# Kernel optimization log

Measured on AMD Instinct MI355X. Metric: run time of the kernel, lower is better.

Reference implementation:

```python
import jax, jax.numpy as jnp
import numpy as np

D_MODEL = 1024
N_HEADS = 16
HEAD_DIM = D_MODEL // N_HEADS  # 64
BASE = 10000.0
MAX_X, MAX_Y, MAX_Z = 32, 32, 8
NEG_INF = -1e9  # stand-in for float('-inf') in masked_fill; identical after softmax


def _split_dims(head_dim):
    n_pairs = head_dim // 2
    px = n_pairs // 3
    py = n_pairs // 3
    pz = n_pairs - px - py
    return px * 2, py * 2, pz * 2


def _cos_sin_table(dim, max_pos):
    # matches RotaryEmbedding3D._register_cache
    inv_freq = 1.0 / (BASE ** (np.arange(0, dim, 2, dtype=np.float32) / dim))
    t = np.arange(max_pos, dtype=np.float32)[:, None] * inv_freq  # [max_pos, dim/2]
    cos = np.repeat(np.cos(t), 2, axis=-1)  # repeat_interleave(2)
    sin = np.repeat(np.sin(t), 2, axis=-1)
    return jnp.asarray(cos), jnp.asarray(sin)


def _rotate_half(x):
    x1 = x[..., ::2]
    x2 = x[..., 1::2]
    return jnp.stack((-x2, x1), axis=-1).reshape(x.shape)


def setup_inputs() -> dict:
    key = jax.random.key(0)
    k1, k2, k3, k4, k5, k6 = jax.random.split(key, 6)
    B, S = 2, 2048
    hidden_states = jax.random.normal(k1, (B, S, D_MODEL), dtype=jnp.float32)
    w_qkv = jax.random.normal(k2, (D_MODEL, 3 * D_MODEL), dtype=jnp.float32) * 0.02
    w_out = jax.random.normal(k3, (D_MODEL, D_MODEL), dtype=jnp.float32) * 0.02
    px = jax.random.randint(k4, (B, S, 1), 0, MAX_X)
    py = jax.random.randint(k5, (B, S, 1), 0, MAX_Y)
    pz = jax.random.randint(k6, (B, S, 1), 0, MAX_Z)
    pos_xyz = jnp.concatenate([px, py, pz], axis=-1).astype(jnp.int64)
    causal_mask = jnp.triu(jnp.ones((S, S), dtype=bool), k=1)[None, None]  # [1,1,S,S]
    return {"hidden_states": hidden_states, "w_qkv": w_qkv, "w_out": w_out,
            "pos_xyz": pos_xyz, "causal_mask": causal_mask}


def reference(hidden_states, w_qkv, w_out, pos_xyz, causal_mask):
    B, S, D = hidden_states.shape
    H, Hd = N_HEADS, HEAD_DIM
    # fused QKV projection
    qkv = hidden_states @ w_qkv  # [B,S,3D]
    qkv = qkv.reshape(B, S, 3, H, Hd).transpose(2, 0, 3, 1, 4)  # [3,B,H,S,Hd]
    q, k, v = qkv[0], qkv[1], qkv[2]
    # 3D RoPE tables and lookups
    dx, dy, dz = _split_dims(Hd)
    cx, sx = _cos_sin_table(dx, MAX_X)
    cy, sy = _cos_sin_table(dy, MAX_Y)
    cz, sz = _cos_sin_table(dz, MAX_Z)
    ix = jnp.clip(pos_xyz[..., 0], 0, MAX_X - 1)
    iy = jnp.clip(pos_xyz[..., 1], 0, MAX_Y - 1)
    iz = jnp.clip(pos_xyz[..., 2], 0, MAX_Z - 1)
    cos = jnp.concatenate([cx[ix], cy[iy], cz[iz]], axis=-1)[:, None]  # [B,1,S,Hd]
    sin = jnp.concatenate([sx[ix], sy[iy], sz[iz]], axis=-1)[:, None]
    q = q * cos + _rotate_half(q) * sin
    k = k * cos + _rotate_half(k) * sin
    # SDPA with causal bias
    scale = Hd ** -0.5
    scores = jnp.einsum('bhqd,bhkd->bhqk', q, k) * scale
    scores = jnp.where(causal_mask, jnp.asarray(NEG_INF, scores.dtype), scores)
    probs = jax.nn.softmax(scores, axis=-1)
    attn = jnp.einsum('bhqk,bhkd->bhqd', probs, v)
    attn = attn.transpose(0, 2, 1, 3).reshape(B, S, D)
    return attn @ w_out
```

## Files before the change

### kernel.cpp

```cpp
#include <hip/hip_runtime.h>
#include <hip/hip_bf16.h>
#include <math.h>

typedef __bf16 bf16;
typedef __bf16 bf16x4 __attribute__((ext_vector_type(4)));
typedef __bf16 bf16x8 __attribute__((ext_vector_type(8)));
typedef float f32x4 __attribute__((ext_vector_type(4)));
typedef int i32x4 __attribute__((ext_vector_type(4)));

#define SEQ 2048
#define NHEADS 16
#define HDIM 64
#define DM 1024
#define QKVW 3072

__device__ __forceinline__ void gload_lds16(const void* g, void* l) {
  __builtin_amdgcn_global_load_lds(
      (const __attribute__((address_space(1))) unsigned int*)g,
      (__attribute__((address_space(3))) unsigned int*)l, 16, 0, 0);
}

__device__ __forceinline__ int pk2(float a, float b) {
  union { __bf16 h; unsigned short u; } ua, ub;
  ua.h = (__bf16)a; ub.h = (__bf16)b;
  return (int)ua.u | ((int)ub.u << 16);
}

__global__ __launch_bounds__(256) void prep(
    const float* __restrict__ hidden, const float* __restrict__ w_qkv,
    const float* __restrict__ w_out, const int* __restrict__ pos,
    bf16* __restrict__ hid_bf, bf16* __restrict__ wqkvT,
    bf16* __restrict__ woutT, float2* __restrict__ tbl) {
  __shared__ float tile[64][65];
  int idx = blockIdx.x, tid = threadIdx.x;
  if (idx < 2048) {
    int i = (idx * 256 + tid) * 8;
    float4 a = *(const float4*)(hidden + i);
    float4 b = *(const float4*)(hidden + i + 4);
    bf16x8 o;
    o[0] = (bf16)a.x; o[1] = (bf16)a.y; o[2] = (bf16)a.z; o[3] = (bf16)a.w;
    o[4] = (bf16)b.x; o[5] = (bf16)b.y; o[6] = (bf16)b.z; o[7] = (bf16)b.w;
    *(bf16x8*)(hid_bf + i) = o;
  } else if (idx < 3072) {
    const float* in; bf16* out; int R, C, t;
    if (idx < 2816) { t = idx - 2048; in = w_qkv; out = wqkvT; R = 1024; C = 3072; }
    else            { t = idx - 2816; in = w_out; out = woutT; R = 1024; C = 1024; }
    int nbx = C >> 6;
    int c0 = (t % nbx) * 64, r0 = (t / nbx) * 64;
    int col = tid & 63, rb = (tid >> 6) * 16;
#pragma unroll
    for (int i = 0; i < 16; ++i)
      tile[rb + i][col] = in[(size_t)(r0 + rb + i) * C + c0 + col];
    __syncthreads();
#pragma unroll
    for (int i = 0; i < 16; ++i)
      out[(size_t)(c0 + rb + i) * R + r0 + col] = (bf16)tile[col][rb + i];
  } else {
    const float LN1E4 = 9.210340371976184f;
    int gi = (idx - 3072) * 256 + tid;
    int m = gi >> 5, pr = gi & 31;
    int axis, d, iloc;
    if (pr < 10)      { axis = 0; d = 20; iloc = pr; }
    else if (pr < 20) { axis = 1; d = 20; iloc = pr - 10; }
    else              { axis = 2; d = 24; iloc = pr - 20; }
    int p = pos[m * 3 + axis];
    int pmax = (axis == 2) ? 7 : 31;
    p = p < 0 ? 0 : (p > pmax ? pmax : p);
    float invf = __expf(-((float)(2 * iloc) / (float)d) * LN1E4);
    float sn, cs;
    __sincosf((float)p * invf, &sn, &cs);
    tbl[gi] = make_float2(cs, sn);
  }
}

__global__ __launch_bounds__(256) void post_qkv(
    bf16* __restrict__ qkv, const float2* __restrict__ tbl,
    bf16* __restrict__ vT) {
  __shared__ bf16 btile[64][65];
  int idx = blockIdx.x, tid = threadIdx.x;
  if (idx < 2048) {
    int gi = idx * 256 + tid;
    int m = gi >> 7, seg = gi & 127;
    bf16* p = qkv + (size_t)m * QKVW + seg * 16;
    bf16x8 a = *(const bf16x8*)p;
    bf16x8 b2 = *(const bf16x8*)(p + 8);
    const float2* t = tbl + m * 32 + (((seg * 16) & 63) >> 1);
#pragma unroll
    for (int j = 0; j < 4; ++j) {
      float2 cs = t[j];
      float e = (float)a[2 * j], o = (float)a[2 * j + 1];
      a[2 * j]     = (bf16)(e * cs.x - o * cs.y);
      a[2 * j + 1] = (bf16)(o * cs.x + e * cs.y);
    }
#pragma unroll
    for (int j = 0; j < 4; ++j) {
      float2 cs = t[4 + j];
      float e = (float)b2[2 * j], o = (float)b2[2 * j + 1];
      b2[2 * j]     = (bf16)(e * cs.x - o * cs.y);
      b2[2 * j + 1] = (bf16)(o * cs.x + e * cs.y);
    }
    *(bf16x8*)p = a;
    *(bf16x8*)(p + 8) = b2;
  } else {
    int t = idx - 2048;
    int s0 = (t & 31) * 64, bh = t >> 5;
    int b = bh >> 4, h = bh & 15;
    const bf16* src = qkv + (size_t)(b * SEQ + s0) * QKVW + 2 * DM + h * 64;
    int col = tid & 63, rb = (tid >> 6) * 16;
#pragma unroll
    for (int i = 0; i < 16; ++i)
      btile[rb + i][col] = src[(size_t)(rb + i) * QKVW + col];
    __syncthreads();
    bf16* dst = vT + (size_t)bh * HDIM * SEQ + s0;
#pragma unroll
    for (int i = 0; i < 16; ++i)
      dst[(size_t)(rb + i) * SEQ + col] = btile[col][rb + i];
  }
}

__global__ __launch_bounds__(256) void gemm_bt(
    const bf16* __restrict__ A, const bf16* __restrict__ Bt,
    bf16* __restrict__ C, int M, int N, int K) {
  __shared__ __align__(16) bf16 a_lds[128 * 32];
  __shared__ __align__(16) bf16 b_lds[128 * 32];
  int tid = threadIdx.x;
  int wave = tid >> 6, lane = tid & 63;
  int quad = lane >> 4, l15 = lane & 15;
  int wm = wave >> 1, wn = wave & 1;

  int flat = blockIdx.y * gridDim.x + blockIdx.x;
  int mband = gridDim.y >> 3;
  int xcd = flat & 7, sidx = flat >> 3;
  int m0 = (xcd * mband + (sidx % mband)) * 128;
  int n0 = (sidx / mband) * 128;

  f32x4 acc[4][4] = {};

  for (int kt = 0; kt < K; kt += 32) {
    __syncthreads();
#pragma unroll
    for (int call = 0; call < 2; ++call) {
      int chunk = call * 256 + tid;
      int row = chunk >> 2, cc = (chunk & 3) * 8;
      gload_lds16(A + (size_t)(m0 + row) * K + kt + cc,
                  (char*)a_lds + call * 4096 + wave * 1024);
      gload_lds16(Bt + (size_t)(n0 + row) * K + kt + cc,
                  (char*)b_lds + call * 4096 + wave * 1024);
    }
    __syncthreads();
    bf16x8 af[4], bfr[4];
#pragma unroll
    for (int i = 0; i < 4; ++i) {
      af[i]  = *(const bf16x8*)(a_lds + (wm * 64 + i * 16 + l15) * 32 + quad * 8);
      bfr[i] = *(const bf16x8*)(b_lds + (wn * 64 + i * 16 + l15) * 32 + quad * 8);
    }
#pragma unroll
    for (int mi = 0; mi < 4; ++mi)
#pragma unroll
      for (int ni = 0; ni < 4; ++ni)
        acc[mi][ni] = __builtin_amdgcn_mfma_f32_16x16x32_bf16(
            af[mi], bfr[ni], acc[mi][ni], 0, 0, 0);
  }

#pragma unroll
  for (int mi = 0; mi < 4; ++mi) {
    int mb = m0 + wm * 64 + mi * 16 + quad * 4;
#pragma unroll
    for (int ni = 0; ni < 4; ++ni) {
      int n = n0 + wn * 64 + ni * 16 + l15;
#pragma unroll
      for (int r = 0; r < 4; ++r)
        C[(size_t)(mb + r) * N + n] = (bf16)acc[mi][ni][r];
    }
  }
}

__global__ __launch_bounds__(256) void gemm_bt64(
    const bf16* __restrict__ A, const bf16* __restrict__ Bt,
    float* __restrict__ C, int M, int N, int K) {
  __shared__ __align__(16) bf16 a_lds[64 * 32];
  __shared__ __align__(16) bf16 b_lds[128 * 32];
  int tid = threadIdx.x;
  int wave = tid >> 6, lane = tid & 63;
  int quad = lane >> 4, l15 = lane & 15;
  int wm = wave >> 1, wn = wave & 1;

  int flat = blockIdx.y * gridDim.x + blockIdx.x;
  int mband = gridDim.y >> 3;
  int xcd = flat & 7, sidx = flat >> 3;
  int m0 = (xcd * mband + (sidx % mband)) * 64;
  int n0 = (sidx / mband) * 128;

  f32x4 acc[2][4] = {};

  for (int kt = 0; kt < K; kt += 32) {
    __syncthreads();
    {
      int row = tid >> 2, cc = (tid & 3) * 8;
      gload_lds16(A + (size_t)(m0 + row) * K + kt + cc,
                  (char*)a_lds + wave * 1024);
    }
#pragma unroll
    for (int call = 0; call < 2; ++call) {
      int chunk = call * 256 + tid;
      int row = chunk >> 2, cc = (chunk & 3) * 8;
      gload_lds16(Bt + (size_t)(n0 + row) * K + kt + cc,
                  (char*)b_lds + call * 4096 + wave * 1024);
    }
    __syncthreads();
    bf16x8 af[2], bfr[4];
#pragma unroll
    for (int i = 0; i < 2; ++i)
      af[i] = *(const bf16x8*)(a_lds + (wm * 32 + i * 16 + l15) * 32 + quad * 8);
#pragma unroll
    for (int i = 0; i < 4; ++i)
      bfr[i] = *(const bf16x8*)(b_lds + (wn * 64 + i * 16 + l15) * 32 + quad * 8);
#pragma unroll
    for (int mi = 0; mi < 2; ++mi)
#pragma unroll
      for (int ni = 0; ni < 4; ++ni)
        acc[mi][ni] = __builtin_amdgcn_mfma_f32_16x16x32_bf16(
            af[mi], bfr[ni], acc[mi][ni], 0, 0, 0);
  }

#pragma unroll
  for (int mi = 0; mi < 2; ++mi) {
    int mb = m0 + wm * 32 + mi * 16 + quad * 4;
#pragma unroll
    for (int ni = 0; ni < 4; ++ni) {
      int n = n0 + wn * 64 + ni * 16 + l15;
#pragma unroll
      for (int r = 0; r < 4; ++r)
        C[(size_t)(mb + r) * N + n] = acc[mi][ni][r];
    }
  }
}

__global__ __launch_bounds__(256) void attn_fwd(
    const bf16* __restrict__ QKV, const bf16* __restrict__ VT,
    bf16* __restrict__ O) {
  __shared__ __align__(16) bf16 k_lds[2][64 * 72];
  __shared__ __align__(16) bf16 v_lds[2][64 * 72];
  const float C2 = 0.18033688011112042f;
  const float C3 = -5.770780163555854f;
  int tid = threadIdx.x;
  int wave = tid >> 6, lane = tid & 63;
  int quad = lane >> 4, l15 = lane & 15;
  int idx = blockIdx.x;
  int bh = idx & 31;
  int g = idx >> 5;
  int qt = (g < 16) ? (31 - g) : (g - 16);
  int q0 = qt * 64;
  int b = bh >> 4, h = bh & 15;
  const bf16* Qb = QKV + (size_t)b * SEQ * QKVW + h * 64;
  const bf16* Kb = Qb + DM;
  const bf16* VTb = VT + (size_t)bh * HDIM * SEQ;

  int qg = q0 + wave * 16 + l15;
  const bf16* qr = Qb + (size_t)qg * QKVW;
  bf16x8 qf0 = *(const bf16x8*)(qr + quad * 8);
  bf16x8 qf1 = *(const bf16x8*)(qr + 32 + quad * 8);

  int r0c = tid >> 3, off0 = (tid & 7) * 8;

  int niter = qt + 1;
  f32x4 oT[4] = {};
  float lsum = 0.f;

  bf16x8 kpre0 = *(const bf16x8*)(Kb + (size_t)r0c * QKVW + off0);
  bf16x8 kpre1 = *(const bf16x8*)(Kb + (size_t)(r0c + 32) * QKVW + off0);
  bf16x8 vpre0 = *(const bf16x8*)(VTb + (size_t)r0c * SEQ + off0);
  bf16x8 vpre1 = *(const bf16x8*)(VTb + (size_t)(r0c + 32) * SEQ + off0);

  for (int tkv = 0; tkv < niter; ++tkv) {
    int kv0 = tkv * 64;
    bf16* kb = k_lds[tkv & 1];
    bf16* vb = v_lds[tkv & 1];
    *(bf16x8*)(kb + r0c * 72 + off0) = kpre0;
    *(bf16x8*)(kb + (r0c + 32) * 72 + off0) = kpre1;
    *(bf16x8*)(vb + r0c * 72 + off0) = vpre0;
    *(bf16x8*)(vb + (r0c + 32) * 72 + off0) = vpre1;
    __syncthreads();
    if (tkv + 1 < niter) {
      int kn = kv0 + 64;
      kpre0 = *(const bf16x8*)(Kb + (size_t)(kn + r0c) * QKVW + off0);
      kpre1 = *(const bf16x8*)(Kb + (size_t)(kn + r0c + 32) * QKVW + off0);
      vpre0 = *(const bf16x8*)(VTb + (size_t)r0c * SEQ + kn + off0);
      vpre1 = *(const bf16x8*)(VTb + (size_t)(r0c + 32) * SEQ + kn + off0);
    }
    f32x4 sT[4];
    __builtin_amdgcn_s_setprio(1);
#pragma unroll
    for (int nt = 0; nt < 4; ++nt) {
      const bf16* kr = kb + (nt * 16 + l15) * 72;
      bf16x8 kf0 = *(const bf16x8*)(kr + quad * 8);
      bf16x8 kf1 = *(const bf16x8*)(kr + 32 + quad * 8);
      f32x4 z = {};
      z = __builtin_amdgcn_mfma_f32_16x16x32_bf16(kf0, qf0, z, 0, 0, 0);
      z = __builtin_amdgcn_mfma_f32_16x16x32_bf16(kf1, qf1, z, 0, 0, 0);
      sT[nt] = z;
    }
    __builtin_amdgcn_s_setprio(0);
    float pv[4][4];
    if (tkv == qt) {
#pragma unroll
      for (int nt = 0; nt < 4; ++nt)
#pragma unroll
        for (int r = 0; r < 4; ++r) {
          float p = __builtin_amdgcn_exp2f(sT[nt][r] * C2 + C3);
          int kvg = kv0 + nt * 16 + 4 * quad + r;
          if (kvg > qg) p = 0.f;
          pv[nt][r] = p;
          lsum += p;
        }
    } else {
#pragma unroll
      for (int nt = 0; nt < 4; ++nt)
#pragma unroll
        for (int r = 0; r < 4; ++r) {
          float p = __builtin_amdgcn_exp2f(sT[nt][r] * C2 + C3);
          pv[nt][r] = p;
          lsum += p;
        }
    }
    i32x4 w0 = {pk2(pv[0][0], pv[0][1]), pk2(pv[0][2], pv[0][3]),
                pk2(pv[1][0], pv[1][1]), pk2(pv[1][2], pv[1][3])};
    i32x4 w1 = {pk2(pv[2][0], pv[2][1]), pk2(pv[2][2], pv[2][3]),
                pk2(pv[3][0], pv[3][1]), pk2(pv[3][2], pv[3][3])};
    bf16x8 pa0 = __builtin_bit_cast(bf16x8, w0);
    bf16x8 pa1 = __builtin_bit_cast(bf16x8, w1);
    __builtin_amdgcn_s_setprio(1);
#pragma unroll
    for (int dt = 0; dt < 4; ++dt) {
      const bf16* vd = vb + (dt * 16 + l15) * 72 + 4 * quad;
      bf16x4 a0 = *(const bf16x4*)(vd);
      bf16x4 a1 = *(const bf16x4*)(vd + 16);
      bf16x8 vf0 = __builtin_shufflevector(a0, a1, 0, 1, 2, 3, 4, 5, 6, 7);
      oT[dt] = __builtin_amdgcn_mfma_f32_16x16x32_bf16(pa0, vf0, oT[dt], 0, 0, 0);
      bf16x4 b0 = *(const bf16x4*)(vd + 32);
      bf16x4 b1 = *(const bf16x4*)(vd + 48);
      bf16x8 vf1 = __builtin_shufflevector(b0, b1, 0, 1, 2, 3, 4, 5, 6, 7);
      oT[dt] = __builtin_amdgcn_mfma_f32_16x16x32_bf16(pa1, vf1, oT[dt], 0, 0, 0);
    }
    __builtin_amdgcn_s_setprio(0);
  }
  float t = lsum;
  t += __shfl_xor(t, 16);
  t += __shfl_xor(t, 32);
#pragma unroll
  for (int r = 0; r < 4; ++r) {
    float Lr = __shfl(t, 4 * quad + r);
    float inv = 1.f / Lr;
    int sq = q0 + wave * 16 + 4 * quad + r;
#pragma unroll
    for (int dt = 0; dt < 4; ++dt)
      O[(size_t)(b * SEQ + sq) * DM + h * HDIM + dt * 16 + l15] =
          (bf16)(oT[dt][r] * inv);
  }
}

extern "C" void kernel_launch(void* const* d_in, const int* in_sizes, int n_in,
                              void* d_out, int out_size, void* d_ws,
                              size_t ws_size, hipStream_t stream) {
  const float* hidden = (const float*)d_in[0];
  const float* w_qkv  = (const float*)d_in[1];
  const float* w_out  = (const float*)d_in[2];
  const int*   pos    = (const int*)d_in[3];
  float* out = (float*)d_out;

  char* ws = (char*)d_ws;
  bf16* wqkvT  = (bf16*)ws;  ws += (size_t)3072 * 1024 * 2;
  bf16* woutT  = (bf16*)ws;  ws += (size_t)1024 * 1024 * 2;
  bf16* hid_bf = (bf16*)ws;  ws += (size_t)4096 * 1024 * 2;
  bf16* qkv_ws = (bf16*)ws;  ws += (size_t)4096 * 3072 * 2;
  bf16* vT_ws  = (bf16*)ws;  ws += (size_t)32 * SEQ * HDIM * 2;
  float2* ropetbl = (float2*)ws;
  bf16* attn_ws = hid_bf;

  prep<<<dim3(3584), 256, 0, stream>>>(hidden, w_qkv, w_out, pos,
                                       hid_bf, wqkvT, woutT, ropetbl);
  gemm_bt<<<dim3(24, 32), 256, 0, stream>>>(
      hid_bf, wqkvT, qkv_ws, 4096, 3072, 1024);
  post_qkv<<<dim3(3072), 256, 0, stream>>>(qkv_ws, ropetbl, vT_ws);
  attn_fwd<<<dim3(1024), 256, 0, stream>>>(qkv_ws, vT_ws, attn_ws);
  gemm_bt64<<<dim3(8, 64), 256, 0, stream>>>(
      attn_ws, woutT, out, 4096, 1024, 1024);
}
```

Measured before the change: 196.1 us.

## Fuse RoPE and V transpose into QKV GEMM epilogue

Removes the separate post_qkv kernel and applies the rotary embedding inside the QKV GEMM epilogue. Paired elements are exchanged with a lane shuffle, and V tiles are written directly in transposed layout as 4-wide bf16 vectors. This saves one launch and a full read and rewrite of the Q/K region plus the V transpose pass. The epilogue becomes heavier: there are per-element table loads, and the transposed stores are strided. RoPE is now applied to fp32 accumulators before the bf16 rounding instead of after it.

```diff
diff --git a/kernel.cpp b/kernel.cpp
--- a/kernel.cpp
+++ b/kernel.cpp
@@ -73,54 +73,10 @@
   }
 }
 
-__global__ __launch_bounds__(256) void post_qkv(
-    bf16* __restrict__ qkv, const float2* __restrict__ tbl,
-    bf16* __restrict__ vT) {
-  __shared__ bf16 btile[64][65];
-  int idx = blockIdx.x, tid = threadIdx.x;
-  if (idx < 2048) {
-    int gi = idx * 256 + tid;
-    int m = gi >> 7, seg = gi & 127;
-    bf16* p = qkv + (size_t)m * QKVW + seg * 16;
-    bf16x8 a = *(const bf16x8*)p;
-    bf16x8 b2 = *(const bf16x8*)(p + 8);
-    const float2* t = tbl + m * 32 + (((seg * 16) & 63) >> 1);
-#pragma unroll
-    for (int j = 0; j < 4; ++j) {
-      float2 cs = t[j];
-      float e = (float)a[2 * j], o = (float)a[2 * j + 1];
-      a[2 * j]     = (bf16)(e * cs.x - o * cs.y);
-      a[2 * j + 1] = (bf16)(o * cs.x + e * cs.y);
-    }
-#pragma unroll
-    for (int j = 0; j < 4; ++j) {
-      float2 cs = t[4 + j];
-      float e = (float)b2[2 * j], o = (float)b2[2 * j + 1];
-      b2[2 * j]     = (bf16)(e * cs.x - o * cs.y);
-      b2[2 * j + 1] = (bf16)(o * cs.x + e * cs.y);
-    }
-    *(bf16x8*)p = a;
-    *(bf16x8*)(p + 8) = b2;
-  } else {
-    int t = idx - 2048;
-    int s0 = (t & 31) * 64, bh = t >> 5;
-    int b = bh >> 4, h = bh & 15;
-    const bf16* src = qkv + (size_t)(b * SEQ + s0) * QKVW + 2 * DM + h * 64;
-    int col = tid & 63, rb = (tid >> 6) * 16;
-#pragma unroll
-    for (int i = 0; i < 16; ++i)
-      btile[rb + i][col] = src[(size_t)(rb + i) * QKVW + col];
-    __syncthreads();
-    bf16* dst = vT + (size_t)bh * HDIM * SEQ + s0;
-#pragma unroll
-    for (int i = 0; i < 16; ++i)
-      dst[(size_t)(rb + i) * SEQ + col] = btile[col][rb + i];
-  }
-}
-
-__global__ __launch_bounds__(256) void gemm_bt(
+__global__ __launch_bounds__(256) void gemm_qkv(
     const bf16* __restrict__ A, const bf16* __restrict__ Bt,
-    bf16* __restrict__ C, int M, int N, int K) {
+    bf16* __restrict__ C, const float2* __restrict__ tbl,
+    bf16* __restrict__ vT, int M, int N, int K) {
   __shared__ __align__(16) bf16 a_lds[128 * 32];
   __shared__ __align__(16) bf16 b_lds[128 * 32];
   int tid = threadIdx.x;
@@ -162,15 +118,40 @@
             af[mi], bfr[ni], acc[mi][ni], 0, 0, 0);
   }
 
-#pragma unroll
-  for (int mi = 0; mi < 4; ++mi) {
-    int mb = m0 + wm * 64 + mi * 16 + quad * 4;
-#pragma unroll
-    for (int ni = 0; ni < 4; ++ni) {
-      int n = n0 + wn * 64 + ni * 16 + l15;
-#pragma unroll
-      for (int r = 0; r < 4; ++r)
-        C[(size_t)(mb + r) * N + n] = (bf16)acc[mi][ni][r];
+  if (n0 >= 2048) {
+    int b = m0 >> 11;
+#pragma unroll
+    for (int mi = 0; mi < 4; ++mi) {
+      int mb = m0 + wm * 64 + mi * 16 + quad * 4;
+      int s0 = mb - b * 2048;
+#pragma unroll
+      for (int ni = 0; ni < 4; ++ni) {
+        int n = n0 + wn * 64 + ni * 16 + l15;
+        int hv = (n - 2048) >> 6, d = n & 63;
+        bf16x4 v4;
+#pragma unroll
+        for (int r = 0; r < 4; ++r) v4[r] = (bf16)acc[mi][ni][r];
+        *(bf16x4*)(vT + ((size_t)(b * 16 + hv) * HDIM + d) * SEQ + s0) = v4;
+      }
+    }
+  } else {
+#pragma unroll
+    for (int mi = 0; mi < 4; ++mi) {
+      int mb = m0 + wm * 64 + mi * 16 + quad * 4;
+#pragma unroll
+      for (int ni = 0; ni < 4; ++ni) {
+        int n = n0 + wn * 64 + ni * 16 + l15;
+        int pr = (n & 63) >> 1;
+        float sgn = (n & 1) ? 1.f : -1.f;
+#pragma unroll
+        for (int r = 0; r < 4; ++r) {
+          float own = acc[mi][ni][r];
+          float par = __shfl_xor(own, 1);
+          int m = mb + r;
+          float2 cs = tbl[m * 32 + pr];
+          C[(size_t)m * N + n] = (bf16)(own * cs.x + sgn * par * cs.y);
+        }
+      }
     }
   }
 }
@@ -379,9 +360,8 @@
 
   prep<<<dim3(3584), 256, 0, stream>>>(hidden, w_qkv, w_out, pos,
                                        hid_bf, wqkvT, woutT, ropetbl);
-  gemm_bt<<<dim3(24, 32), 256, 0, stream>>>(
-      hid_bf, wqkvT, qkv_ws, 4096, 3072, 1024);
-  post_qkv<<<dim3(3072), 256, 0, stream>>>(qkv_ws, ropetbl, vT_ws);
+  gemm_qkv<<<dim3(24, 32), 256, 0, stream>>>(
+      hid_bf, wqkvT, qkv_ws, ropetbl, vT_ws, 4096, 3072, 1024);
   attn_fwd<<<dim3(1024), 256, 0, stream>>>(qkv_ws, vT_ws, attn_ws);
   gemm_bt64<<<dim3(8, 64), 256, 0, stream>>>(
       attn_ws, woutT, out, 4096, 1024, 1024);
```

Measured after the change: 204.8 us. +4.4%, slower.

## Software-pipeline attention loop: overlap QK^T of next tile with softmax/PV of previous

Applied to the files above, without the earlier changes.

Restructures the attention inner loop so that each iteration computes the QK^T scores of the current KV tile while running exp and the PV MFMAs for the previous tile. V fragments are preloaded into registers so the LDS double buffer can be reused safely, and a drain step after the loop handles the final, causally masked tile. The aim is to hide MFMA and exp latency behind each other. It also adds a min-blocks hint of 4 to launch_bounds, which caps registers while the extra live state (sPrev, vpf) raises register pressure and risks spills.

```diff
diff --git a/kernel.cpp b/kernel.cpp
--- a/kernel.cpp
+++ b/kernel.cpp
@@ -236,7 +236,7 @@
   }
 }
 
-__global__ __launch_bounds__(256) void attn_fwd(
+__global__ __launch_bounds__(256, 4) void attn_fwd(
     const bf16* __restrict__ QKV, const bf16* __restrict__ VT,
     bf16* __restrict__ O) {
   __shared__ __align__(16) bf16 k_lds[2][64 * 72];
@@ -267,13 +267,15 @@
   f32x4 oT[4] = {};
   float lsum = 0.f;
 
+  f32x4 sPrev[4];
+  bf16x8 vpf0[4], vpf1[4];
+
   bf16x8 kpre0 = *(const bf16x8*)(Kb + (size_t)r0c * QKVW + off0);
   bf16x8 kpre1 = *(const bf16x8*)(Kb + (size_t)(r0c + 32) * QKVW + off0);
   bf16x8 vpre0 = *(const bf16x8*)(VTb + (size_t)r0c * SEQ + off0);
   bf16x8 vpre1 = *(const bf16x8*)(VTb + (size_t)(r0c + 32) * SEQ + off0);
 
   for (int tkv = 0; tkv < niter; ++tkv) {
-    int kv0 = tkv * 64;
     bf16* kb = k_lds[tkv & 1];
     bf16* vb = v_lds[tkv & 1];
     *(bf16x8*)(kb + r0c * 72 + off0) = kpre0;
@@ -282,13 +284,13 @@
     *(bf16x8*)(vb + (r0c + 32) * 72 + off0) = vpre1;
     __syncthreads();
     if (tkv + 1 < niter) {
-      int kn = kv0 + 64;
+      int kn = tkv * 64 + 64;
       kpre0 = *(const bf16x8*)(Kb + (size_t)(kn + r0c) * QKVW + off0);
       kpre1 = *(const bf16x8*)(Kb + (size_t)(kn + r0c + 32) * QKVW + off0);
       vpre0 = *(const bf16x8*)(VTb + (size_t)r0c * SEQ + kn + off0);
       vpre1 = *(const bf16x8*)(VTb + (size_t)(r0c + 32) * SEQ + kn + off0);
     }
-    f32x4 sT[4];
+    f32x4 sCur[4];
     __builtin_amdgcn_s_setprio(1);
 #pragma unroll
     for (int nt = 0; nt < 4; ++nt) {
@@ -298,51 +300,70 @@
       f32x4 z = {};
       z = __builtin_amdgcn_mfma_f32_16x16x32_bf16(kf0, qf0, z, 0, 0, 0);
       z = __builtin_amdgcn_mfma_f32_16x16x32_bf16(kf1, qf1, z, 0, 0, 0);
-      sT[nt] = z;
+      sCur[nt] = z;
     }
     __builtin_amdgcn_s_setprio(0);
-    float pv[4][4];
-    if (tkv == qt) {
+    if (tkv > 0) {
+      float pv[4][4];
 #pragma unroll
       for (int nt = 0; nt < 4; ++nt)
 #pragma unroll
         for (int r = 0; r < 4; ++r) {
-          float p = __builtin_amdgcn_exp2f(sT[nt][r] * C2 + C3);
-          int kvg = kv0 + nt * 16 + 4 * quad + r;
-          if (kvg > qg) p = 0.f;
+          float p = __builtin_amdgcn_exp2f(sPrev[nt][r] * C2 + C3);
           pv[nt][r] = p;
           lsum += p;
         }
-    } else {
-#pragma unroll
-      for (int nt = 0; nt < 4; ++nt)
-#pragma unroll
-        for (int r = 0; r < 4; ++r) {
-          float p = __builtin_amdgcn_exp2f(sT[nt][r] * C2 + C3);
-          pv[nt][r] = p;
-          lsum += p;
-        }
-    }
+      i32x4 w0 = {pk2(pv[0][0], pv[0][1]), pk2(pv[0][2], pv[0][3]),
+                  pk2(pv[1][0], pv[1][1]), pk2(pv[1][2], pv[1][3])};
+      i32x4 w1 = {pk2(pv[2][0], pv[2][1]), pk2(pv[2][2], pv[2][3]),
+                  pk2(pv[3][0], pv[3][1]), pk2(pv[3][2], pv[3][3])};
+      bf16x8 pa0 = __builtin_bit_cast(bf16x8, w0);
+      bf16x8 pa1 = __builtin_bit_cast(bf16x8, w1);
+      __builtin_amdgcn_s_setprio(1);
+#pragma unroll
+      for (int dt = 0; dt < 4; ++dt) {
+        oT[dt] = __builtin_amdgcn_mfma_f32_16x16x32_bf16(pa0, vpf0[dt], oT[dt], 0, 0, 0);
+        oT[dt] = __builtin_amdgcn_mfma_f32_16x16x32_bf16(pa1, vpf1[dt], oT[dt], 0, 0, 0);
+      }
+      __builtin_amdgcn_s_setprio(0);
+    }
+#pragma unroll
+    for (int dt = 0; dt < 4; ++dt) {
+      const bf16* vd = vb + (dt * 16 + l15) * 72 + 4 * quad;
+      bf16x4 a0 = *(const bf16x4*)(vd);
+      bf16x4 a1 = *(const bf16x4*)(vd + 16);
+      vpf0[dt] = __builtin_shufflevector(a0, a1, 0, 1, 2, 3, 4, 5, 6, 7);
+      bf16x4 b0 = *(const bf16x4*)(vd + 32);
+      bf16x4 b1 = *(const bf16x4*)(vd + 48);
+      vpf1[dt] = __builtin_shufflevector(b0, b1, 0, 1, 2, 3, 4, 5, 6, 7);
+    }
+    sPrev[0] = sCur[0]; sPrev[1] = sCur[1];
+    sPrev[2] = sCur[2]; sPrev[3] = sCur[3];
+  }
+  {
+    int kv0 = (niter - 1) * 64;
+    float pv[4][4];
+#pragma unroll
+    for (int nt = 0; nt < 4; ++nt)
+#pragma unroll
+      for (int r = 0; r < 4; ++r) {
+        float p = __builtin_amdgcn_exp2f(sPrev[nt][r] * C2 + C3);
+        int kvg = kv0 + nt * 16 + 4 * quad + r;
+        if (kvg > qg) p = 0.f;
+        pv[nt][r] = p;
+        lsum += p;
+      }
     i32x4 w0 = {pk2(pv[0][0], pv[0][1]), pk2(pv[0][2], pv[0][3]),
                 pk2(pv[1][0], pv[1][1]), pk2(pv[1][2], pv[1][3])};
     i32x4 w1 = {pk2(pv[2][0], pv[2][1]), pk2(pv[2][2], pv[2][3]),
                 pk2(pv[3][0], pv[3][1]), pk2(pv[3][2], pv[3][3])};
     bf16x8 pa0 = __builtin_bit_cast(bf16x8, w0);
     bf16x8 pa1 = __builtin_bit_cast(bf16x8, w1);
-    __builtin_amdgcn_s_setprio(1);
 #pragma unroll
     for (int dt = 0; dt < 4; ++dt) {
-      const bf16* vd = vb + (dt * 16 + l15) * 72 + 4 * quad;
-      bf16x4 a0 = *(const bf16x4*)(vd);
-      bf16x4 a1 = *(const bf16x4*)(vd + 16);
-      bf16x8 vf0 = __builtin_shufflevector(a0, a1, 0, 1, 2, 3, 4, 5, 6, 7);
-      oT[dt] = __builtin_amdgcn_mfma_f32_16x16x32_bf16(pa0, vf0, oT[dt], 0, 0, 0);
-      bf16x4 b0 = *(const bf16x4*)(vd + 32);
-      bf16x4 b1 = *(const bf16x4*)(vd + 48);
-      bf16x8 vf1 = __builtin_shufflevector(b0, b1, 0, 1, 2, 3, 4, 5, 6, 7);
-      oT[dt] = __builtin_amdgcn_mfma_f32_16x16x32_bf16(pa1, vf1, oT[dt], 0, 0, 0);
-    }
-    __builtin_amdgcn_s_setprio(0);
+      oT[dt] = __builtin_amdgcn_mfma_f32_16x16x32_bf16(pa0, vpf0[dt], oT[dt], 0, 0, 0);
+      oT[dt] = __builtin_amdgcn_mfma_f32_16x16x32_bf16(pa1, vpf1[dt], oT[dt], 0, 0, 0);
+    }
   }
   float t = lsum;
   t += __shfl_xor(t, 16);
```

New measurement: 198.3 us. No clear change (+1.1%).
